# Kernel tuning notes

Hardware: AMD Instinct MI355X
Metric: run time of the kernel (lower is better)

Reference implementation:

```python
import jax, jax.numpy as jnp
import numpy as np

B, S, D, H = 4, 2048, 768, 12
HD = D // H  # head_dim = 64
NEG = 1e10
EPS = 1e-5

def setup_inputs() -> dict:
    key = jax.random.key(0)
    k1, k2, k3 = jax.random.split(key, 3)
    return {
        "context": jax.random.normal(k1, (B, S, D), dtype=jnp.float32),
        "pad_mask": jnp.ones((B, S), dtype=jnp.float32),
        "w_qkv": jax.random.normal(k2, (D, 3 * D), dtype=jnp.float32) * 0.02,
        "w_proj": jax.random.normal(k3, (D, D), dtype=jnp.float32) * (0.02 / np.sqrt(2.0 * 12)),
        "b_proj": jnp.zeros((D,), dtype=jnp.float32),
        "gamma": jnp.ones((D,), dtype=jnp.float32),
        "beta": jnp.zeros((D,), dtype=jnp.float32),
    }

def reference(context, pad_mask, w_qkv, w_proj, b_proj, gamma, beta):
    b, s, d = context.shape
    resid = context
    qkv = context @ w_qkv                       # [B,S,3D]
    q, k, v = jnp.split(qkv, 3, axis=-1)
    # [B,S,D] -> [B,H,S,HD]
    q = q.reshape(b, s, H, HD).transpose(0, 2, 1, 3)
    k = k.reshape(b, s, H, HD).transpose(0, 2, 1, 3)
    v = v.reshape(b, s, H, HD).transpose(0, 2, 1, 3)
    scores = jnp.einsum("bhqd,bhkd->bhqk", q, k) * (1.0 / np.sqrt(HD))
    m = pad_mask[:, None, None, :]              # [B,1,1,S]
    scores = scores * m - (1.0 - m) * NEG       # multiplicative mask + big negative
    attn = jax.nn.softmax(scores, axis=-1)      # dropout is identity at inference
    out = jnp.einsum("bhqk,bhkd->bhqd", attn, v)
    out = out.transpose(0, 2, 1, 3).reshape(b, s, d)
    out = out @ w_proj + b_proj
    x = out + resid
    mu = jnp.mean(x, axis=-1, keepdims=True)
    var = jnp.var(x, axis=-1, keepdims=True)
    return (x - mu) * jax.lax.rsqrt(var + EPS) * gamma + beta
```

## Files before the change

kernel.cpp:

```cpp
#include <hip/hip_runtime.h>

#define BB 4
#define SS 2048
#define DD 768
#define HH 12
#define HDD 64
#define BS (BB*SS)
#define NQKV (3*DD)
#define NEL (BS*DD)

typedef __attribute__((ext_vector_type(8))) __bf16 bf16x8;
typedef __attribute__((ext_vector_type(4))) float fx4;
typedef __attribute__((ext_vector_type(4))) int   ix4;

#define MFMA16(a,b,c) __builtin_amdgcn_mfma_f32_16x16x32_bf16((a),(b),(c),0,0,0)

__device__ __forceinline__ unsigned short f2bf(float f) {
  unsigned u = __builtin_bit_cast(unsigned, f);
  u = (u + 0x7FFFu + ((u >> 16) & 1u)) >> 16;
  return (unsigned short)u;
}
__device__ __forceinline__ unsigned pkbf(float a, float b) {
  unsigned ua = __builtin_bit_cast(unsigned, a);
  unsigned ub = __builtin_bit_cast(unsigned, b);
  return ((ua + 0x8000u) >> 16) | ((ub + 0x8000u) & 0xFFFF0000u);
}

__global__ __launch_bounds__(256) void pack_bf16(const float* __restrict__ x,
                                                 unsigned short* __restrict__ y, int n4) {
  int i = blockIdx.x * 256 + threadIdx.x;
  if (i < n4) {
    float4 v = ((const float4*)x)[i];
    ((uint2*)y)[i] = make_uint2(pkbf(v.x, v.y), pkbf(v.z, v.w));
  }
}

__global__ __launch_bounds__(256) void pack_transpose(const float* __restrict__ w,
                                                      unsigned short* __restrict__ wT,
                                                      int K, int N) {
  __shared__ unsigned short t[32][33];
  int n0 = blockIdx.x * 32, k0 = blockIdx.y * 32;
  int tx = threadIdx.x & 31, ty = threadIdx.x >> 5;
#pragma unroll
  for (int r = ty; r < 32; r += 8)
    t[tx][r] = f2bf(w[(size_t)(k0 + r) * N + n0 + tx]);
  __syncthreads();
#pragma unroll
  for (int r = ty; r < 32; r += 8)
    wT[(size_t)(n0 + r) * K + k0 + tx] = t[r][tx];
}

__global__ __launch_bounds__(256) void gemm_qkv_k(const unsigned short* __restrict__ Wt,
                                                  const unsigned short* __restrict__ X,
                                                  unsigned short* __restrict__ Qo,
                                                  unsigned short* __restrict__ Ko,
                                                  unsigned short* __restrict__ Vto) {
  __shared__ unsigned short As[128 * 32];
  __shared__ unsigned short Bs[128 * 32];
  const int tid = threadIdx.x;
  const int w = tid >> 6, lane = tid & 63, quad = lane >> 4, l16 = lane & 15;
  const int m0 = blockIdx.y << 7;
  const int n0 = blockIdx.x << 7;
  const int wm = (w & 1) * 64, wn = (w >> 1) * 64;
  fx4 acc[4][4];
#pragma unroll
  for (int i = 0; i < 4; ++i)
#pragma unroll
    for (int c = 0; c < 4; ++c) acc[i][c] = (fx4){0.f, 0.f, 0.f, 0.f};

  const int c0 = tid, c1 = 256 + tid;
  const unsigned short* Ag0 = Wt + (size_t)(m0 + (c0 >> 2)) * DD + (c0 & 3) * 8;
  const unsigned short* Ag1 = Wt + (size_t)(m0 + (c1 >> 2)) * DD + (c1 & 3) * 8;
  const unsigned short* Bg0 = X + (size_t)(n0 + (c0 >> 2)) * DD + (c0 & 3) * 8;
  const unsigned short* Bg1 = X + (size_t)(n0 + (c1 >> 2)) * DD + (c1 & 3) * 8;

  ix4 ra0 = *(const ix4*)Ag0;
  ix4 ra1 = *(const ix4*)Ag1;
  ix4 rb0 = *(const ix4*)Bg0;
  ix4 rb1 = *(const ix4*)Bg1;

  for (int k0 = 0; k0 < DD; k0 += 32) {
    __syncthreads();
    *(ix4*)((char*)As + c0 * 16) = ra0;
    *(ix4*)((char*)As + c1 * 16) = ra1;
    *(ix4*)((char*)Bs + c0 * 16) = rb0;
    *(ix4*)((char*)Bs + c1 * 16) = rb1;
    __syncthreads();
    if (k0 + 32 < DD) {
      ra0 = *(const ix4*)(Ag0 + k0 + 32);
      ra1 = *(const ix4*)(Ag1 + k0 + 32);
      rb0 = *(const ix4*)(Bg0 + k0 + 32);
      rb1 = *(const ix4*)(Bg1 + k0 + 32);
    }
    bf16x8 af[4], bf[4];
#pragma unroll
    for (int i = 0; i < 4; ++i) af[i] = *(const bf16x8*)&As[(wm + i * 16 + l16) * 32 + quad * 8];
#pragma unroll
    for (int c = 0; c < 4; ++c) bf[c] = *(const bf16x8*)&Bs[(wn + c * 16 + l16) * 32 + quad * 8];
#pragma unroll
    for (int i = 0; i < 4; ++i)
#pragma unroll
      for (int c = 0; c < 4; ++c) acc[i][c] = MFMA16(af[i], bf[c], acc[i][c]);
  }

  const int which = m0 / DD;
#pragma unroll
  for (int i = 0; i < 4; ++i) {
    int fb = m0 + wm + i * 16 + quad * 4;
    int d = fb - which * DD;
    int h = d >> 6, hd = d & 63;
#pragma unroll
    for (int c = 0; c < 4; ++c) {
      int srow = n0 + wn + c * 16 + l16;
      int b = srow >> 11, s = srow & (SS - 1);
      if (which == 0) {
        uint2 v = make_uint2(pkbf(acc[i][c][0], acc[i][c][1]), pkbf(acc[i][c][2], acc[i][c][3]));
        *(uint2*)&Qo[((size_t)(b * HH + h) * SS + s) * HDD + hd] = v;
      } else if (which == 1) {
        uint2 v = make_uint2(pkbf(acc[i][c][0], acc[i][c][1]), pkbf(acc[i][c][2], acc[i][c][3]));
        *(uint2*)&Ko[((size_t)(b * HH + h) * SS + s) * HDD + hd] = v;
      } else {
#pragma unroll
        for (int r = 0; r < 4; ++r)
          Vto[((size_t)(b * HH + h) * HDD + hd + r) * SS + s] = f2bf(acc[i][c][r]);
      }
    }
  }
}

__global__ __launch_bounds__(256) void gemm_proj_k(const unsigned short* __restrict__ Wt,
                                                   const unsigned short* __restrict__ X,
                                                   const float* __restrict__ ctx,
                                                   const float* __restrict__ bproj,
                                                   float* __restrict__ xf) {
  __shared__ unsigned short As[128 * 32];
  __shared__ unsigned short Bs[128 * 32];
  const int tid = threadIdx.x;
  const int w = tid >> 6, lane = tid & 63, quad = lane >> 4, l16 = lane & 15;
  const int m0 = blockIdx.y << 7;
  const int n0 = blockIdx.x << 7;
  const int wm = (w & 1) * 64, wn = (w >> 1) * 64;
  fx4 acc[4][4];
#pragma unroll
  for (int i = 0; i < 4; ++i)
#pragma unroll
    for (int c = 0; c < 4; ++c) acc[i][c] = (fx4){0.f, 0.f, 0.f, 0.f};

  const int c0 = tid, c1 = 256 + tid;
  const unsigned short* Ag0 = Wt + (size_t)(m0 + (c0 >> 2)) * DD + (c0 & 3) * 8;
  const unsigned short* Ag1 = Wt + (size_t)(m0 + (c1 >> 2)) * DD + (c1 & 3) * 8;
  const unsigned short* Bg0 = X + (size_t)(n0 + (c0 >> 2)) * DD + (c0 & 3) * 8;
  const unsigned short* Bg1 = X + (size_t)(n0 + (c1 >> 2)) * DD + (c1 & 3) * 8;

  ix4 ra0 = *(const ix4*)Ag0;
  ix4 ra1 = *(const ix4*)Ag1;
  ix4 rb0 = *(const ix4*)Bg0;
  ix4 rb1 = *(const ix4*)Bg1;

  for (int k0 = 0; k0 < DD; k0 += 32) {
    __syncthreads();
    *(ix4*)((char*)As + c0 * 16) = ra0;
    *(ix4*)((char*)As + c1 * 16) = ra1;
    *(ix4*)((char*)Bs + c0 * 16) = rb0;
    *(ix4*)((char*)Bs + c1 * 16) = rb1;
    __syncthreads();
    if (k0 + 32 < DD) {
      ra0 = *(const ix4*)(Ag0 + k0 + 32);
      ra1 = *(const ix4*)(Ag1 + k0 + 32);
      rb0 = *(const ix4*)(Bg0 + k0 + 32);
      rb1 = *(const ix4*)(Bg1 + k0 + 32);
    }
    bf16x8 af[4], bf[4];
#pragma unroll
    for (int i = 0; i < 4; ++i) af[i] = *(const bf16x8*)&As[(wm + i * 16 + l16) * 32 + quad * 8];
#pragma unroll
    for (int c = 0; c < 4; ++c) bf[c] = *(const bf16x8*)&Bs[(wn + c * 16 + l16) * 32 + quad * 8];
#pragma unroll
    for (int i = 0; i < 4; ++i)
#pragma unroll
      for (int c = 0; c < 4; ++c) acc[i][c] = MFMA16(af[i], bf[c], acc[i][c]);
  }

#pragma unroll
  for (int i = 0; i < 4; ++i) {
    int fb = m0 + wm + i * 16 + quad * 4;
    float4 bp = *(const float4*)&bproj[fb];
#pragma unroll
    for (int c = 0; c < 4; ++c) {
      int srow = n0 + wn + c * 16 + l16;
      float4 cx = *(const float4*)&ctx[(size_t)srow * DD + fb];
      float4 r;
      r.x = acc[i][c][0] + bp.x + cx.x;
      r.y = acc[i][c][1] + bp.y + cx.y;
      r.z = acc[i][c][2] + bp.z + cx.z;
      r.w = acc[i][c][3] + bp.w + cx.w;
      *(float4*)&xf[(size_t)srow * DD + fb] = r;
    }
  }
}

__global__ __launch_bounds__(256) void attn_k(const unsigned short* __restrict__ Q,
                                              const unsigned short* __restrict__ K,
                                              const unsigned short* __restrict__ Vt,
                                              const float* __restrict__ mask,
                                              unsigned short* __restrict__ O) {
  __shared__ unsigned short Ks[64 * 64];
  __shared__ unsigned short Vts[64 * 64];
  const int tid = threadIdx.x;
  const int w = tid >> 6, lane = tid & 63;
  const int quad = lane >> 4, l16 = lane & 15;
  const int bh = blockIdx.y;
  const int b = bh / HH, h = bh - b * HH;
  const int q0 = blockIdx.x << 7;
  const unsigned short* Qb = Q + (size_t)bh * (SS * HDD);
  const unsigned short* Kb = K + (size_t)bh * (SS * HDD);
  const unsigned short* Vtb = Vt + (size_t)bh * (SS * HDD);
  const float* mb = mask + b * SS;

  bf16x8 qf[2][2];
#pragma unroll
  for (int qi = 0; qi < 2; ++qi)
#pragma unroll
    for (int f = 0; f < 2; ++f)
      qf[qi][f] = *(const bf16x8*)&Qb[(size_t)(q0 + w * 32 + qi * 16 + l16) * HDD + f * 32 + quad * 8];

  fx4 o[2][4];
#pragma unroll
  for (int qi = 0; qi < 2; ++qi)
#pragma unroll
    for (int ht = 0; ht < 4; ++ht) o[qi][ht] = (fx4){0.f, 0.f, 0.f, 0.f};
  float lsum[2] = {0.f, 0.f};

  const int cA = tid, cB = 256 + tid;
  const int rA = cA >> 3, pA = (cA & 7) ^ (rA & 7);
  const int rB = cB >> 3, pB = (cB & 7) ^ (rB & 7);

  ix4 rk0 = *(const ix4*)&Kb[(size_t)rA * HDD + pA * 8];
  ix4 rk1 = *(const ix4*)&Kb[(size_t)rB * HDD + pB * 8];
  ix4 rv0 = *(const ix4*)&Vtb[(size_t)rA * SS + pA * 8];
  ix4 rv1 = *(const ix4*)&Vtb[(size_t)rB * SS + pB * 8];

  for (int k0 = 0; k0 < SS; k0 += 64) {
    __syncthreads();
    *(ix4*)((char*)Ks + cA * 16) = rk0;
    *(ix4*)((char*)Ks + cB * 16) = rk1;
    *(ix4*)((char*)Vts + cA * 16) = rv0;
    *(ix4*)((char*)Vts + cB * 16) = rv1;
    __syncthreads();
    if (k0 + 64 < SS) {
      int kn = k0 + 64;
      rk0 = *(const ix4*)&Kb[(size_t)(kn + rA) * HDD + pA * 8];
      rk1 = *(const ix4*)&Kb[(size_t)(kn + rB) * HDD + pB * 8];
      rv0 = *(const ix4*)&Vtb[(size_t)rA * SS + kn + pA * 8];
      rv1 = *(const ix4*)&Vtb[(size_t)rB * SS + kn + pB * 8];
    }

    float4 mq[4];
#pragma unroll
    for (int kt = 0; kt < 4; ++kt)
      mq[kt] = *(const float4*)&mb[k0 + kt * 16 + quad * 4];

    bf16x8 kf[4][2];
#pragma unroll
    for (int kt = 0; kt < 4; ++kt) {
      int row = kt * 16 + l16;
      int rx = row & 7;
#pragma unroll
      for (int f = 0; f < 2; ++f)
        kf[kt][f] = *(const bf16x8*)&Ks[row * 64 + ((f * 4 + quad) ^ rx) * 8];
    }
    bf16x8 vf[4][2];
#pragma unroll
    for (int ht = 0; ht < 4; ++ht) {
      int row = ht * 16 + l16;
      int rx = row & 7;
#pragma unroll
      for (int f = 0; f < 2; ++f) {
        int dc0 = (f * 4 + (quad >> 1)) ^ rx;
        int dc1 = (f * 4 + 2 + (quad >> 1)) ^ rx;
        uint2 lo = *(const uint2*)((const char*)Vts + row * 128 + dc0 * 16 + (quad & 1) * 8);
        uint2 hi = *(const uint2*)((const char*)Vts + row * 128 + dc1 * 16 + (quad & 1) * 8);
        ix4 vv = (ix4){(int)lo.x, (int)lo.y, (int)hi.x, (int)hi.y};
        vf[ht][f] = __builtin_bit_cast(bf16x8, vv);
      }
    }

#pragma unroll
    for (int qi = 0; qi < 2; ++qi) {
      fx4 sc[4];
#pragma unroll
      for (int kt = 0; kt < 4; ++kt) {
        fx4 s = (fx4){0.f, 0.f, 0.f, 0.f};
        s = MFMA16(kf[kt][0], qf[qi][0], s);
        s = MFMA16(kf[kt][1], qf[qi][1], s);
        sc[kt] = s;
      }
      unsigned pk[4][2];
      float ls = 0.f;
#pragma unroll
      for (int kt = 0; kt < 4; ++kt) {
        float p[4];
#pragma unroll
        for (int r = 0; r < 4; ++r) {
          float mv = ((const float*)&mq[kt])[r];
          p[r] = __expf(sc[kt][r] * (0.125f * mv) - (1.f - mv) * 1e10f);
          ls += p[r];
        }
        pk[kt][0] = pkbf(p[0], p[1]);
        pk[kt][1] = pkbf(p[2], p[3]);
      }
      lsum[qi] += ls;
      ix4 p0 = (ix4){(int)pk[0][0], (int)pk[0][1], (int)pk[1][0], (int)pk[1][1]};
      ix4 p1 = (ix4){(int)pk[2][0], (int)pk[2][1], (int)pk[3][0], (int)pk[3][1]};
      bf16x8 pf0 = __builtin_bit_cast(bf16x8, p0);
      bf16x8 pf1 = __builtin_bit_cast(bf16x8, p1);
#pragma unroll
      for (int ht = 0; ht < 4; ++ht) {
        o[qi][ht] = MFMA16(vf[ht][0], pf0, o[qi][ht]);
        o[qi][ht] = MFMA16(vf[ht][1], pf1, o[qi][ht]);
      }
    }
  }

#pragma unroll
  for (int qi = 0; qi < 2; ++qi) {
    float t = lsum[qi];
    t += __shfl_xor(t, 16);
    t += __shfl_xor(t, 32);
    float inv = 1.f / fmaxf(t, 1e-30f);
    int sq = q0 + w * 32 + qi * 16 + l16;
    unsigned short* orow = O + ((size_t)(b * SS + sq)) * DD + h * HDD;
#pragma unroll
    for (int ht = 0; ht < 4; ++ht) {
      uint2 v = make_uint2(pkbf(o[qi][ht][0] * inv, o[qi][ht][1] * inv),
                           pkbf(o[qi][ht][2] * inv, o[qi][ht][3] * inv));
      *(uint2*)&orow[ht * 16 + quad * 4] = v;
    }
  }
}

__global__ __launch_bounds__(256) void ln_k(const float* __restrict__ x,
                                            const float* __restrict__ gamma,
                                            const float* __restrict__ beta,
                                            float* __restrict__ out) {
  const int row = blockIdx.x;
  const float* xr = x + (size_t)row * DD;
  const int t = threadIdx.x;
  float v0 = xr[t], v1 = xr[t + 256], v2 = xr[t + 512];
  float s = v0 + v1 + v2;
  float ss = v0 * v0 + v1 * v1 + v2 * v2;
#pragma unroll
  for (int d = 32; d > 0; d >>= 1) {
    s += __shfl_down(s, d);
    ss += __shfl_down(ss, d);
  }
  __shared__ float sh[10];
  int wv = t >> 6, lane = t & 63;
  if (lane == 0) { sh[wv] = s; sh[4 + wv] = ss; }
  __syncthreads();
  if (t == 0) {
    float S = sh[0] + sh[1] + sh[2] + sh[3];
    float SSm = sh[4] + sh[5] + sh[6] + sh[7];
    float mu = S * (1.0f / DD);
    float var = SSm * (1.0f / DD) - mu * mu;
    sh[8] = mu;
    sh[9] = rsqrtf(var + 1e-5f);
  }
  __syncthreads();
  float mu = sh[8], rstd = sh[9];
  out[(size_t)row * DD + t]       = (v0 - mu) * rstd * gamma[t]       + beta[t];
  out[(size_t)row * DD + t + 256] = (v1 - mu) * rstd * gamma[t + 256] + beta[t + 256];
  out[(size_t)row * DD + t + 512] = (v2 - mu) * rstd * gamma[t + 512] + beta[t + 512];
}

extern "C" void kernel_launch(void* const* d_in, const int* in_sizes, int n_in,
                              void* d_out, int out_size, void* d_ws, size_t ws_size,
                              hipStream_t stream) {
  (void)in_sizes; (void)n_in; (void)out_size; (void)ws_size;
  const float* ctx   = (const float*)d_in[0];
  const float* mask  = (const float*)d_in[1];
  const float* wqkv  = (const float*)d_in[2];
  const float* wproj = (const float*)d_in[3];
  const float* bproj = (const float*)d_in[4];
  const float* gamma = (const float*)d_in[5];
  const float* beta  = (const float*)d_in[6];
  float* out = (float*)d_out;

  char* p = (char*)d_ws;
  unsigned short* Xbf = (unsigned short*)p; p += (size_t)NEL * 2;
  unsigned short* Qw  = (unsigned short*)p; p += (size_t)NEL * 2;
  unsigned short* Kw  = (unsigned short*)p; p += (size_t)NEL * 2;
  unsigned short* Vtw = (unsigned short*)p; p += (size_t)NEL * 2;
  unsigned short* Ao  = (unsigned short*)p; p += (size_t)NEL * 2;
  unsigned short* WqkvT  = (unsigned short*)p; p += (size_t)DD * NQKV * 2;
  unsigned short* WprojT = (unsigned short*)p; p += (size_t)DD * DD * 2;
  float* xf = (float*)Qw;

  pack_bf16<<<NEL / 4 / 256, 256, 0, stream>>>(ctx, Xbf, NEL / 4);
  pack_transpose<<<dim3(NQKV / 32, DD / 32), 256, 0, stream>>>(wqkv, WqkvT, DD, NQKV);
  pack_transpose<<<dim3(DD / 32, DD / 32), 256, 0, stream>>>(wproj, WprojT, DD, DD);
  gemm_qkv_k<<<dim3(BS / 128, NQKV / 128), 256, 0, stream>>>(WqkvT, Xbf, Qw, Kw, Vtw);
  attn_k<<<dim3(SS / 128, BB * HH), 256, 0, stream>>>(Qw, Kw, Vtw, mask, Ao);
  gemm_proj_k<<<dim3(BS / 128, DD / 128), 256, 0, stream>>>(WprojT, Ao, ctx, bproj, xf);
  ln_k<<<BS, 256, 0, stream>>>(xf, gamma, beta, out);
}
```

Before: 276.5 us.

## Double-buffer LDS tiles in GEMMs and attention, fuse prep kernels, use exp2

The QKV GEMM, projection GEMM and attention kernels now use two shared-memory buffers. Each iteration writes the next tile into the other buffer after its MFMAs, so one barrier per iteration replaces two. The three preparation kernels (activation bf16 pack and two weight transposes) are merged into one launch selected by block index. The attention softmax folds the mask and scale into a single fma feeding exp2f. In exchange, LDS use doubles, which may lower occupancy.

```diff
diff --git a/kernel.cpp b/kernel.cpp
--- a/kernel.cpp
+++ b/kernel.cpp
@@ -9,6 +9,10 @@
 #define NQKV (3*DD)
 #define NEL (BS*DD)
 
+#define NB_PACK 6144
+#define NB_TQKV 1728
+#define NB_TPRJ 576
+
 typedef __attribute__((ext_vector_type(8))) __bf16 bf16x8;
 typedef __attribute__((ext_vector_type(4))) float fx4;
 typedef __attribute__((ext_vector_type(4))) int   ix4;
@@ -26,28 +30,38 @@
   return ((ua + 0x8000u) >> 16) | ((ub + 0x8000u) & 0xFFFF0000u);
 }
 
-__global__ __launch_bounds__(256) void pack_bf16(const float* __restrict__ x,
-                                                 unsigned short* __restrict__ y, int n4) {
-  int i = blockIdx.x * 256 + threadIdx.x;
-  if (i < n4) {
-    float4 v = ((const float4*)x)[i];
-    ((uint2*)y)[i] = make_uint2(pkbf(v.x, v.y), pkbf(v.z, v.w));
-  }
-}
-
-__global__ __launch_bounds__(256) void pack_transpose(const float* __restrict__ w,
-                                                      unsigned short* __restrict__ wT,
-                                                      int K, int N) {
+__global__ __launch_bounds__(256) void prep_k(const float* __restrict__ ctx,
+                                              unsigned short* __restrict__ Xbf,
+                                              const float* __restrict__ wqkv,
+                                              unsigned short* __restrict__ WqkvT,
+                                              const float* __restrict__ wproj,
+                                              unsigned short* __restrict__ WprojT) {
+  const int bid = blockIdx.x;
+  const int tid = threadIdx.x;
+  if (bid < NB_PACK) {
+    int i = bid * 256 + tid;
+    float4 v = ((const float4*)ctx)[i];
+    ((uint2*)Xbf)[i] = make_uint2(pkbf(v.x, v.y), pkbf(v.z, v.w));
+    return;
+  }
   __shared__ unsigned short t[32][33];
-  int n0 = blockIdx.x * 32, k0 = blockIdx.y * 32;
-  int tx = threadIdx.x & 31, ty = threadIdx.x >> 5;
+  const float* w; unsigned short* wT; int N, bx, by;
+  if (bid < NB_PACK + NB_TQKV) {
+    int b2 = bid - NB_PACK;
+    w = wqkv; wT = WqkvT; N = NQKV; bx = b2 % 72; by = b2 / 72;
+  } else {
+    int b3 = bid - NB_PACK - NB_TQKV;
+    w = wproj; wT = WprojT; N = DD; bx = b3 % 24; by = b3 / 24;
+  }
+  int n0 = bx * 32, k0 = by * 32;
+  int tx = tid & 31, ty = tid >> 5;
 #pragma unroll
   for (int r = ty; r < 32; r += 8)
     t[tx][r] = f2bf(w[(size_t)(k0 + r) * N + n0 + tx]);
   __syncthreads();
 #pragma unroll
   for (int r = ty; r < 32; r += 8)
-    wT[(size_t)(n0 + r) * K + k0 + tx] = t[r][tx];
+    wT[(size_t)(n0 + r) * DD + k0 + tx] = t[r][tx];
 }
 
 __global__ __launch_bounds__(256) void gemm_qkv_k(const unsigned short* __restrict__ Wt,
@@ -55,8 +69,8 @@
                                                   unsigned short* __restrict__ Qo,
                                                   unsigned short* __restrict__ Ko,
                                                   unsigned short* __restrict__ Vto) {
-  __shared__ unsigned short As[128 * 32];
-  __shared__ unsigned short Bs[128 * 32];
+  __shared__ unsigned short As[2][128 * 32];
+  __shared__ unsigned short Bs[2][128 * 32];
   const int tid = threadIdx.x;
   const int w = tid >> 6, lane = tid & 63, quad = lane >> 4, l16 = lane & 15;
   const int m0 = blockIdx.y << 7;
@@ -78,15 +92,16 @@
   ix4 ra1 = *(const ix4*)Ag1;
   ix4 rb0 = *(const ix4*)Bg0;
   ix4 rb1 = *(const ix4*)Bg1;
+  *(ix4*)((char*)As[0] + c0 * 16) = ra0;
+  *(ix4*)((char*)As[0] + c1 * 16) = ra1;
+  *(ix4*)((char*)Bs[0] + c0 * 16) = rb0;
+  *(ix4*)((char*)Bs[0] + c1 * 16) = rb1;
+  __syncthreads();
 
   for (int k0 = 0; k0 < DD; k0 += 32) {
-    __syncthreads();
-    *(ix4*)((char*)As + c0 * 16) = ra0;
-    *(ix4*)((char*)As + c1 * 16) = ra1;
-    *(ix4*)((char*)Bs + c0 * 16) = rb0;
-    *(ix4*)((char*)Bs + c1 * 16) = rb1;
-    __syncthreads();
-    if (k0 + 32 < DD) {
+    const int cur = (k0 >> 5) & 1;
+    const bool more = (k0 + 32 < DD);
+    if (more) {
       ra0 = *(const ix4*)(Ag0 + k0 + 32);
       ra1 = *(const ix4*)(Ag1 + k0 + 32);
       rb0 = *(const ix4*)(Bg0 + k0 + 32);
@@ -94,13 +109,20 @@
     }
     bf16x8 af[4], bf[4];
 #pragma unroll
-    for (int i = 0; i < 4; ++i) af[i] = *(const bf16x8*)&As[(wm + i * 16 + l16) * 32 + quad * 8];
-#pragma unroll
-    for (int c = 0; c < 4; ++c) bf[c] = *(const bf16x8*)&Bs[(wn + c * 16 + l16) * 32 + quad * 8];
+    for (int i = 0; i < 4; ++i) af[i] = *(const bf16x8*)&As[cur][(wm + i * 16 + l16) * 32 + quad * 8];
+#pragma unroll
+    for (int c = 0; c < 4; ++c) bf[c] = *(const bf16x8*)&Bs[cur][(wn + c * 16 + l16) * 32 + quad * 8];
 #pragma unroll
     for (int i = 0; i < 4; ++i)
 #pragma unroll
       for (int c = 0; c < 4; ++c) acc[i][c] = MFMA16(af[i], bf[c], acc[i][c]);
+    if (more) {
+      *(ix4*)((char*)As[cur ^ 1] + c0 * 16) = ra0;
+      *(ix4*)((char*)As[cur ^ 1] + c1 * 16) = ra1;
+      *(ix4*)((char*)Bs[cur ^ 1] + c0 * 16) = rb0;
+      *(ix4*)((char*)Bs[cur ^ 1] + c1 * 16) = rb1;
+    }
+    __syncthreads();
   }
 
   const int which = m0 / DD;
@@ -133,8 +155,8 @@
                                                    const float* __restrict__ ctx,
                                                    const float* __restrict__ bproj,
                                                    float* __restrict__ xf) {
-  __shared__ unsigned short As[128 * 32];
-  __shared__ unsigned short Bs[128 * 32];
+  __shared__ unsigned short As[2][128 * 32];
+  __shared__ unsigned short Bs[2][128 * 32];
   const int tid = threadIdx.x;
   const int w = tid >> 6, lane = tid & 63, quad = lane >> 4, l16 = lane & 15;
   const int m0 = blockIdx.y << 7;
@@ -156,15 +178,16 @@
   ix4 ra1 = *(const ix4*)Ag1;
   ix4 rb0 = *(const ix4*)Bg0;
   ix4 rb1 = *(const ix4*)Bg1;
+  *(ix4*)((char*)As[0] + c0 * 16) = ra0;
+  *(ix4*)((char*)As[0] + c1 * 16) = ra1;
+  *(ix4*)((char*)Bs[0] + c0 * 16) = rb0;
+  *(ix4*)((char*)Bs[0] + c1 * 16) = rb1;
+  __syncthreads();
 
   for (int k0 = 0; k0 < DD; k0 += 32) {
-    __syncthreads();
-    *(ix4*)((char*)As + c0 * 16) = ra0;
-    *(ix4*)((char*)As + c1 * 16) = ra1;
-    *(ix4*)((char*)Bs + c0 * 16) = rb0;
-    *(ix4*)((char*)Bs + c1 * 16) = rb1;
-    __syncthreads();
-    if (k0 + 32 < DD) {
+    const int cur = (k0 >> 5) & 1;
+    const bool more = (k0 + 32 < DD);
+    if (more) {
       ra0 = *(const ix4*)(Ag0 + k0 + 32);
       ra1 = *(const ix4*)(Ag1 + k0 + 32);
       rb0 = *(const ix4*)(Bg0 + k0 + 32);
@@ -172,13 +195,20 @@
     }
     bf16x8 af[4], bf[4];
 #pragma unroll
-    for (int i = 0; i < 4; ++i) af[i] = *(const bf16x8*)&As[(wm + i * 16 + l16) * 32 + quad * 8];
-#pragma unroll
-    for (int c = 0; c < 4; ++c) bf[c] = *(const bf16x8*)&Bs[(wn + c * 16 + l16) * 32 + quad * 8];
+    for (int i = 0; i < 4; ++i) af[i] = *(const bf16x8*)&As[cur][(wm + i * 16 + l16) * 32 + quad * 8];
+#pragma unroll
+    for (int c = 0; c < 4; ++c) bf[c] = *(const bf16x8*)&Bs[cur][(wn + c * 16 + l16) * 32 + quad * 8];
 #pragma unroll
     for (int i = 0; i < 4; ++i)
 #pragma unroll
       for (int c = 0; c < 4; ++c) acc[i][c] = MFMA16(af[i], bf[c], acc[i][c]);
+    if (more) {
+      *(ix4*)((char*)As[cur ^ 1] + c0 * 16) = ra0;
+      *(ix4*)((char*)As[cur ^ 1] + c1 * 16) = ra1;
+      *(ix4*)((char*)Bs[cur ^ 1] + c0 * 16) = rb0;
+      *(ix4*)((char*)Bs[cur ^ 1] + c1 * 16) = rb1;
+    }
+    __syncthreads();
   }
 
 #pragma unroll
@@ -204,8 +234,8 @@
                                               const unsigned short* __restrict__ Vt,
                                               const float* __restrict__ mask,
                                               unsigned short* __restrict__ O) {
-  __shared__ unsigned short Ks[64 * 64];
-  __shared__ unsigned short Vts[64 * 64];
+  __shared__ unsigned short Ks[2][64 * 64];
+  __shared__ unsigned short Vts[2][64 * 64];
   const int tid = threadIdx.x;
   const int w = tid >> 6, lane = tid & 63;
   const int quad = lane >> 4, l16 = lane & 15;
@@ -217,6 +247,9 @@
   const unsigned short* Vtb = Vt + (size_t)bh * (SS * HDD);
   const float* mb = mask + b * SS;
 
+  const float C2 = 0.125f * 1.44269504089f;
+  const float OFF2 = 1.0e10f * 1.44269504089f;
+
   bf16x8 qf[2][2];
 #pragma unroll
   for (int qi = 0; qi < 2; ++qi)
@@ -239,26 +272,34 @@
   ix4 rk1 = *(const ix4*)&Kb[(size_t)rB * HDD + pB * 8];
   ix4 rv0 = *(const ix4*)&Vtb[(size_t)rA * SS + pA * 8];
   ix4 rv1 = *(const ix4*)&Vtb[(size_t)rB * SS + pB * 8];
+  *(ix4*)((char*)Ks[0] + cA * 16) = rk0;
+  *(ix4*)((char*)Ks[0] + cB * 16) = rk1;
+  *(ix4*)((char*)Vts[0] + cA * 16) = rv0;
+  *(ix4*)((char*)Vts[0] + cB * 16) = rv1;
+  __syncthreads();
 
   for (int k0 = 0; k0 < SS; k0 += 64) {
-    __syncthreads();
-    *(ix4*)((char*)Ks + cA * 16) = rk0;
-    *(ix4*)((char*)Ks + cB * 16) = rk1;
-    *(ix4*)((char*)Vts + cA * 16) = rv0;
-    *(ix4*)((char*)Vts + cB * 16) = rv1;
-    __syncthreads();
-    if (k0 + 64 < SS) {
+    const int cur = (k0 >> 6) & 1;
+    const bool more = (k0 + 64 < SS);
+    if (more) {
       int kn = k0 + 64;
       rk0 = *(const ix4*)&Kb[(size_t)(kn + rA) * HDD + pA * 8];
       rk1 = *(const ix4*)&Kb[(size_t)(kn + rB) * HDD + pB * 8];
       rv0 = *(const ix4*)&Vtb[(size_t)rA * SS + kn + pA * 8];
       rv1 = *(const ix4*)&Vtb[(size_t)rB * SS + kn + pB * 8];
     }
-
-    float4 mq[4];
-#pragma unroll
-    for (int kt = 0; kt < 4; ++kt)
-      mq[kt] = *(const float4*)&mb[k0 + kt * 16 + quad * 4];
+    const unsigned short* KsC = Ks[cur];
+    const unsigned short* VtsC = Vts[cur];
+
+    float4 offn[4];
+#pragma unroll
+    for (int kt = 0; kt < 4; ++kt) {
+      float4 mv = *(const float4*)&mb[k0 + kt * 16 + quad * 4];
+      offn[kt].x = fmaf(OFF2, mv.x, -OFF2);
+      offn[kt].y = fmaf(OFF2, mv.y, -OFF2);
+      offn[kt].z = fmaf(OFF2, mv.z, -OFF2);
+      offn[kt].w = fmaf(OFF2, mv.w, -OFF2);
+    }
 
     bf16x8 kf[4][2];
 #pragma unroll
@@ -267,7 +308,7 @@
       int rx = row & 7;
 #pragma unroll
       for (int f = 0; f < 2; ++f)
-        kf[kt][f] = *(const bf16x8*)&Ks[row * 64 + ((f * 4 + quad) ^ rx) * 8];
+        kf[kt][f] = *(const bf16x8*)&KsC[row * 64 + ((f * 4 + quad) ^ rx) * 8];
     }
     bf16x8 vf[4][2];
 #pragma unroll
@@ -278,8 +319,8 @@
       for (int f = 0; f < 2; ++f) {
         int dc0 = (f * 4 + (quad >> 1)) ^ rx;
         int dc1 = (f * 4 + 2 + (quad >> 1)) ^ rx;
-        uint2 lo = *(const uint2*)((const char*)Vts + row * 128 + dc0 * 16 + (quad & 1) * 8);
-        uint2 hi = *(const uint2*)((const char*)Vts + row * 128 + dc1 * 16 + (quad & 1) * 8);
+        uint2 lo = *(const uint2*)((const char*)VtsC + row * 128 + dc0 * 16 + (quad & 1) * 8);
+        uint2 hi = *(const uint2*)((const char*)VtsC + row * 128 + dc1 * 16 + (quad & 1) * 8);
         ix4 vv = (ix4){(int)lo.x, (int)lo.y, (int)hi.x, (int)hi.y};
         vf[ht][f] = __builtin_bit_cast(bf16x8, vv);
       }
@@ -299,13 +340,12 @@
       float ls = 0.f;
 #pragma unroll
       for (int kt = 0; kt < 4; ++kt) {
+        const float* offr = (const float*)&offn[kt];
         float p[4];
 #pragma unroll
-        for (int r = 0; r < 4; ++r) {
-          float mv = ((const float*)&mq[kt])[r];
-          p[r] = __expf(sc[kt][r] * (0.125f * mv) - (1.f - mv) * 1e10f);
-          ls += p[r];
-        }
+        for (int r = 0; r < 4; ++r)
+          p[r] = exp2f(fmaf(sc[kt][r], C2, offr[r]));
+        ls += (p[0] + p[1]) + (p[2] + p[3]);
         pk[kt][0] = pkbf(p[0], p[1]);
         pk[kt][1] = pkbf(p[2], p[3]);
       }
@@ -320,6 +360,14 @@
         o[qi][ht] = MFMA16(vf[ht][1], pf1, o[qi][ht]);
       }
     }
+
+    if (more) {
+      *(ix4*)((char*)Ks[cur ^ 1] + cA * 16) = rk0;
+      *(ix4*)((char*)Ks[cur ^ 1] + cB * 16) = rk1;
+      *(ix4*)((char*)Vts[cur ^ 1] + cA * 16) = rv0;
+      *(ix4*)((char*)Vts[cur ^ 1] + cB * 16) = rv1;
+    }
+    __syncthreads();
   }
 
 #pragma unroll
@@ -396,9 +444,7 @@
   unsigned short* WprojT = (unsigned short*)p; p += (size_t)DD * DD * 2;
   float* xf = (float*)Qw;
 
-  pack_bf16<<<NEL / 4 / 256, 256, 0, stream>>>(ctx, Xbf, NEL / 4);
-  pack_transpose<<<dim3(NQKV / 32, DD / 32), 256, 0, stream>>>(wqkv, WqkvT, DD, NQKV);
-  pack_transpose<<<dim3(DD / 32, DD / 32), 256, 0, stream>>>(wproj, WprojT, DD, DD);
+  prep_k<<<NB_PACK + NB_TQKV + NB_TPRJ, 256, 0, stream>>>(ctx, Xbf, wqkv, WqkvT, wproj, WprojT);
   gemm_qkv_k<<<dim3(BS / 128, NQKV / 128), 256, 0, stream>>>(WqkvT, Xbf, Qw, Kw, Vtw);
   attn_k<<<dim3(SS / 128, BB * HH), 256, 0, stream>>>(Qw, Kw, Vtw, mask, Ao);
   gemm_proj_k<<<dim3(BS / 128, DD / 128), 256, 0, stream>>>(WprojT, Ao, ctx, bproj, xf);
```

Result: no change. 279.9 us (+1.2%).
